# Kernel optimization log

Measured on AMD Instinct MI355X. Metric: run time of the kernel, lower is better.

Reference implementation:

```python
import jax, jax.numpy as jnp
import numpy as np

FRAME_LENGTH = 512
HOP_LENGTH = 256
ENERGY_THRESHOLD = 0.01
SAMPLE_RATE = 16000
SILENCE_FRAMES = int(0.3 * SAMPLE_RATE / HOP_LENGTH)      # 18
MIN_SPEECH_FRAMES = int(0.1 * SAMPLE_RATE / HOP_LENGTH)   # 6


def setup_inputs() -> dict:
    key = jax.random.key(0)
    waveform = jax.random.normal(key, (32, 960000), dtype=jnp.float32)
    return {"waveform": waveform}


def _compute_energy(waveform):
    # (B, S) -> (B, T): short-time mean-square energy, full frames only
    n = waveform.shape[-1]
    num_frames = max(1, (n - FRAME_LENGTH) // HOP_LENGTH + 1)
    idx = jnp.arange(num_frames)[:, None] * HOP_LENGTH + jnp.arange(FRAME_LENGTH)[None, :]
    frames = waveform[:, idx]                     # (B, T, F)
    return jnp.mean(frames * frames, axis=-1)


def _threshold(e):
    # torch.quantile(non_zero, 0.2) with linear interpolation; fallback to fixed threshold
    n = e.shape[0]
    s = jnp.sort(e)
    nzero = jnp.sum(s <= 0)          # number of entries excluded by (> 0)
    nz = n - nzero                   # count of positive entries
    pos = 0.2 * (nz - 1).astype(jnp.float32)
    lo = jnp.floor(pos).astype(jnp.int32)
    hi = jnp.ceil(pos).astype(jnp.int32)
    frac = pos - lo.astype(jnp.float32)
    ilo = jnp.clip(nzero + lo, 0, n - 1)
    ihi = jnp.clip(nzero + hi, 0, n - 1)
    q = s[ilo] * (1.0 - frac) + s[ihi] * frac
    return jnp.where(nz > 0, q, jnp.float32(ENERGY_THRESHOLD))


def _vad_one(e):
    # Faithful scan-based version of the per-frame hysteresis state machine.
    n = e.shape[0]
    m = e > _threshold(e)

    def step(state, xs):
        in_sp, start, sil = state
        t, mt = xs
        start2 = jnp.where(mt & ~in_sp, t, start)
        sil2 = jnp.where(mt, jnp.int32(0), jnp.where(in_sp, sil + 1, sil))
        closed = (~mt) & in_sp & (sil2 >= SILENCE_FRAMES)
        end = t - sil2  # matches original: end = t - silence_count (exclusive)
        in_sp2 = jnp.where(mt, True, jnp.where(closed, False, in_sp))
        return (in_sp2, start2, sil2), (closed, start2, end)

    init = (jnp.bool_(False), jnp.int32(0), jnp.int32(0))
    (in_sp_f, start_f, _), (closed, starts, ends) = jax.lax.scan(
        step, init, (jnp.arange(n, dtype=jnp.int32), m))

    # trailing open segment -> (start, n)
    starts = jnp.concatenate([starts, start_f[None]])
    ends = jnp.concatenate([ends, jnp.full((1,), n, dtype=jnp.int32)])
    valid = jnp.concatenate([closed, in_sp_f[None]])
    valid = valid & ((ends - starts) >= MIN_SPEECH_FRAMES)

    # mark mask[start:end] = True via +1/-1 diff then cumsum (RLE)
    sentinel = n + 1
    idx_s = jnp.where(valid, jnp.clip(starts, 0, n), sentinel)
    idx_e = jnp.where(valid, jnp.clip(ends, 0, n), sentinel)
    d = jnp.zeros(n + 2, dtype=jnp.int32)
    d = d.at[idx_s].add(1).at[idx_e].add(-1)
    return jnp.cumsum(d)[:n] > 0


def reference(waveform):
    energy = _compute_energy(waveform)     # (B, T)
    return jax.vmap(_vad_one)(energy)      # (B, T) bool VAD mask
```

## Files before the change

kernel.cpp:

```cpp
#include <hip/hip_runtime.h>

#define NFRAMES 3749
#define NBLOCKS 3750
#define NSAMP   960000
#define NBATCH  32
#define NWORDS  59
#define SILENCE_FRAMES 18
#define MIN_SPEECH_FRAMES 6
#define MAXSEG  256

__global__ __launch_bounds__(256) void vad_block_sums(const float* __restrict__ wav,
                                                      double* __restrict__ bs) {
    int tid = threadIdx.x;
    const float* p = wav + (size_t)blockIdx.x * 4096 + tid * 16;
    double acc = 0.0;
    #pragma unroll
    for (int i = 0; i < 4; ++i) {
        float4 v = *(const float4*)(p + i * 4);
        acc += (double)(v.x * v.x);
        acc += (double)(v.y * v.y);
        acc += (double)(v.z * v.z);
        acc += (double)(v.w * v.w);
    }
    #pragma unroll
    for (int m = 1; m < 16; m <<= 1)
        acc += __shfl_xor(acc, m, 64);
    if ((tid & 15) == 0)
        bs[(size_t)blockIdx.x * 16 + (tid >> 4)] = acc;
}

__global__ __launch_bounds__(256) void vad_finish(const double* __restrict__ bs,
                                                  int* __restrict__ out) {
    __shared__ float eng[NFRAMES];
    __shared__ int hist4[4][256];
    __shared__ unsigned long long mw[NWORDS];
    __shared__ unsigned long long sw[NWORDS];
    __shared__ unsigned long long lw[NWORDS];
    __shared__ unsigned long long Sw[NWORDS];
    __shared__ unsigned long long Ew[NWORDS];
    __shared__ int wbS[NWORDS], wbL[NWORDS];
    __shared__ int startpos[MAXSEG], lastpos[MAXSEG];
    __shared__ int nzero_sh, nseg_sh;
    __shared__ unsigned sel_prefix_sh;
    __shared__ int sel_k_sh;
    __shared__ int cLE_sh;
    __shared__ unsigned minGT_sh;
    __shared__ float thr_sh;

    int b = blockIdx.x;
    int tid = threadIdx.x;
    int lane = tid & 63, wv = tid >> 6;
    const double* row = bs + (size_t)b * NBLOCKS;

    if (tid == 0) nzero_sh = 0;
    __syncthreads();

    unsigned ub[15];
    int nel = 0, myzero = 0;
    #pragma unroll
    for (int i = 0; i < 15; ++i) {
        int t = tid + (i << 8);
        if (t < NFRAMES) {
            double s = row[t] + row[t + 1];
            float e = (float)(s * (1.0 / 512.0));
            eng[t] = e;
            ub[nel++] = __float_as_uint(e);
            if (e <= 0.0f) myzero++;
        }
    }
    if (myzero) atomicAdd(&nzero_sh, myzero);
    __syncthreads();

    int nzero = nzero_sh;
    int nz = NFRAMES - nzero;

    if (nz > 0) {
        float pos = 0.2f * (float)(nz - 1);
        int lo = (int)floorf(pos), hi = (int)ceilf(pos);
        int rank_lo = min(max(nzero + lo, 0), NFRAMES - 1);
        int rank_hi = min(max(nzero + hi, 0), NFRAMES - 1);

        for (int i = tid; i < 1024; i += 256) ((int*)hist4)[i] = 0;
        if (tid == 0) { sel_prefix_sh = 0u; sel_k_sh = rank_lo; }
        __syncthreads();

        for (int shift = 24; shift >= 0; shift -= 8) {
            unsigned pref = sel_prefix_sh;
            unsigned pmask = (shift == 24) ? 0u : (0xFFFFFFFFu << (shift + 8));
            for (int j = 0; j < nel; ++j) {
                unsigned u = ub[j];
                if ((u & pmask) == (pref & pmask))
                    atomicAdd(&hist4[wv][(u >> shift) & 255], 1);
            }
            __syncthreads();
            if (wv == 0) {
                int bin0 = lane << 2;
                int4 h0 = *(const int4*)&hist4[0][bin0];
                int4 h1 = *(const int4*)&hist4[1][bin0];
                int4 h2 = *(const int4*)&hist4[2][bin0];
                int4 h3 = *(const int4*)&hist4[3][bin0];
                int h[4];
                h[0] = h0.x + h1.x + h2.x + h3.x;
                h[1] = h0.y + h1.y + h2.y + h3.y;
                h[2] = h0.z + h1.z + h2.z + h3.z;
                h[3] = h0.w + h1.w + h2.w + h3.w;
                int tot = h[0] + h[1] + h[2] + h[3];
                int inc = tot;
                #pragma unroll
                for (int off = 1; off < 64; off <<= 1) {
                    int y = __shfl_up(inc, off, 64);
                    if (lane >= off) inc += y;
                }
                int run = inc - tot;
                int k = sel_k_sh;
                #pragma unroll
                for (int j = 0; j < 4; ++j) {
                    if (k >= run && k < run + h[j]) {
                        sel_prefix_sh = pref | ((unsigned)(bin0 + j) << shift);
                        sel_k_sh = k - run;
                    }
                    run += h[j];
                }
            }
            __syncthreads();
            if (shift > 0) {
                for (int i = tid; i < 1024; i += 256) ((int*)hist4)[i] = 0;
            }
            __syncthreads();
        }

        unsigned vb = sel_prefix_sh;

        if (rank_hi != rank_lo) {
            if (tid == 0) { cLE_sh = 0; minGT_sh = 0xFFFFFFFFu; }
            __syncthreads();
            int c = 0;
            unsigned mg = 0xFFFFFFFFu;
            for (int j = 0; j < nel; ++j) {
                unsigned u = ub[j];
                if (u <= vb) c++;
                else mg = min(mg, u);
            }
            #pragma unroll
            for (int off = 32; off > 0; off >>= 1) {
                c += __shfl_xor(c, off, 64);
                mg = min(mg, (unsigned)__shfl_xor((int)mg, off, 64));
            }
            if (lane == 0) {
                atomicAdd(&cLE_sh, c);
                atomicMin(&minGT_sh, mg);
            }
            __syncthreads();
        }

        if (tid == 0) {
            float vlo = __uint_as_float(vb);
            float vhi;
            if (rank_hi == rank_lo) vhi = vlo;
            else vhi = (cLE_sh >= rank_lo + 2) ? vlo : __uint_as_float(minGT_sh);
            float frac = pos - (float)lo;
            thr_sh = vlo * (1.0f - frac) + vhi * frac;
        }
    } else {
        if (tid == 0) thr_sh = 0.01f;
    }
    __syncthreads();
    float thr = thr_sh;

    for (int wi = wv; wi < NWORDS; wi += 4) {
        int t = (wi << 6) + lane;
        bool p = (t < NFRAMES) && (eng[t] > thr);
        unsigned long long bm = __ballot(p);
        if (lane == 0) mw[wi] = bm;
    }
    __syncthreads();

    for (int wi = wv; wi < NWORDS; wi += 4) {
        unsigned long long W  = mw[wi];
        unsigned long long Wm = (wi > 0) ? mw[wi - 1] : 0ull;
        unsigned long long Wp = (wi + 1 < NWORDS) ? mw[wi + 1] : 0ull;
        int l = lane;
        bool mt = (W >> l) & 1ull;
        bool prev_any, next_any;
        if (l >= 18) {
            prev_any = ((W >> (l - 18)) & 0x3FFFFull) != 0ull;
        } else {
            unsigned long long lowpart = W & ((1ull << l) - 1ull);
            unsigned long long hipart  = Wm >> (46 + l);
            prev_any = (lowpart | hipart) != 0ull;
        }
        if (l <= 45) {
            next_any = ((W >> (l + 1)) & 0x3FFFFull) != 0ull;
        } else {
            unsigned long long a  = (l < 63) ? (W >> (l + 1)) : 0ull;
            unsigned long long bb = Wp & ((1ull << (l - 45)) - 1ull);
            next_any = (a | bb) != 0ull;
        }
        unsigned long long bS = __ballot(mt && !prev_any);
        unsigned long long bL = __ballot(mt && !next_any);
        if (lane == 0) { sw[wi] = bS; lw[wi] = bL; }
    }
    __syncthreads();

    if (tid < NWORDS) {
        int cS = 0, cL = 0;
        for (int j = 0; j < tid; ++j) { cS += __popcll(sw[j]); cL += __popcll(lw[j]); }
        wbS[tid] = cS; wbL[tid] = cL;
        if (tid == NWORDS - 1) nseg_sh = cS + __popcll(sw[tid]);
    }
    __syncthreads();

    for (int wi = wv; wi < NWORDS; wi += 4) {
        unsigned long long wS = sw[wi], wL = lw[wi];
        int t = (wi << 6) + lane;
        unsigned long long lmask = (1ull << lane) - 1ull;
        if ((wS >> lane) & 1ull) startpos[wbS[wi] + __popcll(wS & lmask)] = t;
        if ((wL >> lane) & 1ull) lastpos[wbL[wi] + __popcll(wL & lmask)] = t;
    }
    for (int wi = tid; wi < NWORDS; wi += 256) { Sw[wi] = 0ull; Ew[wi] = 0ull; }
    __syncthreads();

    int nseg = nseg_sh;
    for (int k = tid; k < nseg; k += 256) {
        int s = startpos[k], L = lastpos[k];
        int e = (L >= NFRAMES - SILENCE_FRAMES) ? NFRAMES : L;
        if (e - s >= MIN_SPEECH_FRAMES) {
            atomicOr(&Sw[s >> 6], 1ull << (s & 63));
            atomicOr(&Ew[e >> 6], 1ull << (e & 63));
        }
    }
    __syncthreads();

    if (tid < NWORDS) {
        int cS = 0, cE = 0;
        for (int j = 0; j < tid; ++j) { cS += __popcll(Sw[j]); cE += __popcll(Ew[j]); }
        wbS[tid] = cS; wbL[tid] = cE;
    }
    __syncthreads();

    int* orow = out + (size_t)b * NFRAMES;
    for (int wi = wv; wi < NWORDS; wi += 4) {
        unsigned long long wS2 = Sw[wi], wE2 = Ew[wi];
        int t = (wi << 6) + lane;
        unsigned long long ile = (lane == 63) ? ~0ull : ((1ull << (lane + 1)) - 1ull);
        int cS = wbS[wi] + __popcll(wS2 & ile);
        int cE = wbL[wi] + __popcll(wE2 & ile);
        if (t < NFRAMES) orow[t] = (cS > cE) ? 1 : 0;
    }
}

extern "C" void kernel_launch(void* const* d_in, const int* in_sizes, int n_in,
                              void* d_out, int out_size, void* d_ws, size_t ws_size,
                              hipStream_t stream) {
    const float* wav = (const float*)d_in[0];
    int* out = (int*)d_out;
    double* bs = (double*)d_ws;

    vad_block_sums<<<(NBATCH * NSAMP) / 4096, 256, 0, stream>>>(wav, bs);
    vad_finish<<<NBATCH, 256, 0, stream>>>(bs, out);
}
```

Baseline: 197.5 us.

## Coalesce block-sum loads and widen finish kernel with per-pass histograms

The block-sum kernel now reads float4s in a fully coalesced stride across the block and reduces each 256-sample block with a full-wave shuffle. The finish kernel moves to 512 threads and keeps energies in registers instead of shared memory. It gives each radix-select pass its own per-wave histogram, so the zeroing barriers go away, and aggregates atomics when all lanes in a wave hit the same bin. Serial popcount prefix loops become wave-level scans. The intent is to cut latency in the single-block-per-batch finish stage and improve memory coalescing, at the cost of more shared memory and extra ballots per radix-select element.

```diff
diff --git a/kernel.cpp b/kernel.cpp
--- a/kernel.cpp
+++ b/kernel.cpp
@@ -12,27 +12,24 @@
 __global__ __launch_bounds__(256) void vad_block_sums(const float* __restrict__ wav,
                                                       double* __restrict__ bs) {
     int tid = threadIdx.x;
-    const float* p = wav + (size_t)blockIdx.x * 4096 + tid * 16;
-    double acc = 0.0;
+    int w = tid >> 6, lane = tid & 63;
+    const float4* q = (const float4*)(wav + (size_t)blockIdx.x * 4096);
     #pragma unroll
     for (int i = 0; i < 4; ++i) {
-        float4 v = *(const float4*)(p + i * 4);
-        acc += (double)(v.x * v.x);
-        acc += (double)(v.y * v.y);
-        acc += (double)(v.z * v.z);
-        acc += (double)(v.w * v.w);
-    }
-    #pragma unroll
-    for (int m = 1; m < 16; m <<= 1)
-        acc += __shfl_xor(acc, m, 64);
-    if ((tid & 15) == 0)
-        bs[(size_t)blockIdx.x * 16 + (tid >> 4)] = acc;
+        float4 v = q[(i << 8) + tid];
+        double a = (double)(v.x * v.x) + (double)(v.y * v.y)
+                 + (double)(v.z * v.z) + (double)(v.w * v.w);
+        #pragma unroll
+        for (int m = 1; m < 64; m <<= 1)
+            a += __shfl_xor(a, m, 64);
+        if (lane == 0)
+            bs[(size_t)blockIdx.x * 16 + (i << 2) + w] = a;
+    }
 }
 
-__global__ __launch_bounds__(256) void vad_finish(const double* __restrict__ bs,
+__global__ __launch_bounds__(512) void vad_finish(const double* __restrict__ bs,
                                                   int* __restrict__ out) {
-    __shared__ float eng[NFRAMES];
-    __shared__ int hist4[4][256];
+    __shared__ __attribute__((aligned(16))) int hist[4][8][256];
     __shared__ unsigned long long mw[NWORDS];
     __shared__ unsigned long long sw[NWORDS];
     __shared__ unsigned long long lw[NWORDS];
@@ -52,23 +49,29 @@
     int lane = tid & 63, wv = tid >> 6;
     const double* row = bs + (size_t)b * NBLOCKS;
 
-    if (tid == 0) nzero_sh = 0;
-    __syncthreads();
-
-    unsigned ub[15];
-    int nel = 0, myzero = 0;
-    #pragma unroll
-    for (int i = 0; i < 15; ++i) {
-        int t = tid + (i << 8);
+    if (tid == 0) { nzero_sh = 0; sel_prefix_sh = 0u; cLE_sh = 0; minGT_sh = 0xFFFFFFFFu; }
+    #pragma unroll
+    for (int i = 0; i < 4; ++i)
+        ((int4*)hist)[(i << 9) + tid] = make_int4(0, 0, 0, 0);
+
+    unsigned ub[8];
+    int myzero = 0;
+    #pragma unroll
+    for (int i = 0; i < 8; ++i) {
+        int t = tid + (i << 9);
+        unsigned u = 0xFFFFFFFFu;
         if (t < NFRAMES) {
             double s = row[t] + row[t + 1];
             float e = (float)(s * (1.0 / 512.0));
-            eng[t] = e;
-            ub[nel++] = __float_as_uint(e);
+            u = __float_as_uint(e);
             if (e <= 0.0f) myzero++;
         }
-    }
-    if (myzero) atomicAdd(&nzero_sh, myzero);
+        ub[i] = u;
+    }
+    #pragma unroll
+    for (int m = 1; m < 64; m <<= 1)
+        myzero += __shfl_xor(myzero, m, 64);
+    if (lane == 0 && myzero) atomicAdd(&nzero_sh, myzero);
     __syncthreads();
 
     int nzero = nzero_sh;
@@ -79,32 +82,40 @@
         int lo = (int)floorf(pos), hi = (int)ceilf(pos);
         int rank_lo = min(max(nzero + lo, 0), NFRAMES - 1);
         int rank_hi = min(max(nzero + hi, 0), NFRAMES - 1);
-
-        for (int i = tid; i < 1024; i += 256) ((int*)hist4)[i] = 0;
-        if (tid == 0) { sel_prefix_sh = 0u; sel_k_sh = rank_lo; }
-        __syncthreads();
-
-        for (int shift = 24; shift >= 0; shift -= 8) {
+        if (tid == 0) sel_k_sh = rank_lo;
+
+        int pno = 0;
+        for (int shift = 24; shift >= 0; shift -= 8, ++pno) {
             unsigned pref = sel_prefix_sh;
             unsigned pmask = (shift == 24) ? 0u : (0xFFFFFFFFu << (shift + 8));
-            for (int j = 0; j < nel; ++j) {
+            int* hw = hist[pno][wv];
+            #pragma unroll
+            for (int j = 0; j < 8; ++j) {
                 unsigned u = ub[j];
-                if ((u & pmask) == (pref & pmask))
-                    atomicAdd(&hist4[wv][(u >> shift) & 255], 1);
+                bool act = ((int)u >= 0) && ((u & pmask) == (pref & pmask));
+                unsigned long long ball = __ballot(act);
+                if (ball != 0ull) {
+                    unsigned bin = (u >> shift) & 255u;
+                    int leader = (int)__ffsll(ball) - 1;
+                    unsigned fbin = (unsigned)__shfl((int)bin, leader, 64);
+                    unsigned long long same = __ballot(act && (bin == fbin));
+                    if (same == ball) {
+                        if (lane == leader) atomicAdd(&hw[fbin], (int)__popcll(ball));
+                    } else if (act) {
+                        atomicAdd(&hw[bin], 1);
+                    }
+                }
             }
             __syncthreads();
             if (wv == 0) {
                 int bin0 = lane << 2;
-                int4 h0 = *(const int4*)&hist4[0][bin0];
-                int4 h1 = *(const int4*)&hist4[1][bin0];
-                int4 h2 = *(const int4*)&hist4[2][bin0];
-                int4 h3 = *(const int4*)&hist4[3][bin0];
-                int h[4];
-                h[0] = h0.x + h1.x + h2.x + h3.x;
-                h[1] = h0.y + h1.y + h2.y + h3.y;
-                h[2] = h0.z + h1.z + h2.z + h3.z;
-                h[3] = h0.w + h1.w + h2.w + h3.w;
-                int tot = h[0] + h[1] + h[2] + h[3];
+                int h0 = 0, h1 = 0, h2 = 0, h3 = 0;
+                #pragma unroll
+                for (int c = 0; c < 8; ++c) {
+                    int4 hc = *(const int4*)&hist[pno][c][bin0];
+                    h0 += hc.x; h1 += hc.y; h2 += hc.z; h3 += hc.w;
+                }
+                int tot = h0 + h1 + h2 + h3;
                 int inc = tot;
                 #pragma unroll
                 for (int off = 1; off < 64; off <<= 1) {
@@ -113,33 +124,31 @@
                 }
                 int run = inc - tot;
                 int k = sel_k_sh;
+                int hh[4] = {h0, h1, h2, h3};
                 #pragma unroll
-                for (int j = 0; j < 4; ++j) {
-                    if (k >= run && k < run + h[j]) {
-                        sel_prefix_sh = pref | ((unsigned)(bin0 + j) << shift);
+                for (int j2 = 0; j2 < 4; ++j2) {
+                    if (k >= run && k < run + hh[j2]) {
+                        sel_prefix_sh = pref | ((unsigned)(bin0 + j2) << shift);
                         sel_k_sh = k - run;
                     }
-                    run += h[j];
+                    run += hh[j2];
                 }
             }
             __syncthreads();
-            if (shift > 0) {
-                for (int i = tid; i < 1024; i += 256) ((int*)hist4)[i] = 0;
-            }
-            __syncthreads();
         }
 
         unsigned vb = sel_prefix_sh;
 
         if (rank_hi != rank_lo) {
-            if (tid == 0) { cLE_sh = 0; minGT_sh = 0xFFFFFFFFu; }
-            __syncthreads();
             int c = 0;
             unsigned mg = 0xFFFFFFFFu;
-            for (int j = 0; j < nel; ++j) {
+            #pragma unroll
+            for (int j = 0; j < 8; ++j) {
                 unsigned u = ub[j];
-                if (u <= vb) c++;
-                else mg = min(mg, u);
+                if ((int)u >= 0) {
+                    if (u <= vb) c++;
+                    else mg = min(mg, u);
+                }
             }
             #pragma unroll
             for (int off = 32; off > 0; off >>= 1) {
@@ -167,15 +176,17 @@
     __syncthreads();
     float thr = thr_sh;
 
-    for (int wi = wv; wi < NWORDS; wi += 4) {
-        int t = (wi << 6) + lane;
-        bool p = (t < NFRAMES) && (eng[t] > thr);
+    #pragma unroll
+    for (int i = 0; i < 8; ++i) {
+        unsigned u = ub[i];
+        bool p = ((int)u >= 0) && (__uint_as_float(u) > thr);
         unsigned long long bm = __ballot(p);
-        if (lane == 0) mw[wi] = bm;
-    }
-    __syncthreads();
-
-    for (int wi = wv; wi < NWORDS; wi += 4) {
+        int wi = wv + (i << 3);
+        if (lane == 0 && wi < NWORDS) mw[wi] = bm;
+    }
+    __syncthreads();
+
+    for (int wi = wv; wi < NWORDS; wi += 8) {
         unsigned long long W  = mw[wi];
         unsigned long long Wm = (wi > 0) ? mw[wi - 1] : 0ull;
         unsigned long long Wp = (wi + 1 < NWORDS) ? mw[wi + 1] : 0ull;
@@ -202,26 +213,34 @@
     }
     __syncthreads();
 
-    if (tid < NWORDS) {
-        int cS = 0, cL = 0;
-        for (int j = 0; j < tid; ++j) { cS += __popcll(sw[j]); cL += __popcll(lw[j]); }
-        wbS[tid] = cS; wbL[tid] = cL;
-        if (tid == NWORDS - 1) nseg_sh = cS + __popcll(sw[tid]);
-    }
-    __syncthreads();
-
-    for (int wi = wv; wi < NWORDS; wi += 4) {
+    if (wv < 2) {
+        const unsigned long long* src = (wv == 0) ? sw : lw;
+        unsigned long long w_ = (lane < NWORDS) ? src[lane] : 0ull;
+        int c = __popcll(w_);
+        int inc = c;
+        #pragma unroll
+        for (int off = 1; off < 64; off <<= 1) {
+            int y = __shfl_up(inc, off, 64);
+            if (lane >= off) inc += y;
+        }
+        int* dst = (wv == 0) ? wbS : wbL;
+        if (lane < NWORDS) dst[lane] = inc - c;
+        if (wv == 0 && lane == NWORDS - 1) nseg_sh = inc;
+    }
+    __syncthreads();
+
+    for (int wi = wv; wi < NWORDS; wi += 8) {
         unsigned long long wS = sw[wi], wL = lw[wi];
         int t = (wi << 6) + lane;
         unsigned long long lmask = (1ull << lane) - 1ull;
         if ((wS >> lane) & 1ull) startpos[wbS[wi] + __popcll(wS & lmask)] = t;
         if ((wL >> lane) & 1ull) lastpos[wbL[wi] + __popcll(wL & lmask)] = t;
     }
-    for (int wi = tid; wi < NWORDS; wi += 256) { Sw[wi] = 0ull; Ew[wi] = 0ull; }
+    for (int wi = tid; wi < NWORDS; wi += 512) { Sw[wi] = 0ull; Ew[wi] = 0ull; }
     __syncthreads();
 
     int nseg = nseg_sh;
-    for (int k = tid; k < nseg; k += 256) {
+    for (int k = tid; k < nseg; k += 512) {
         int s = startpos[k], L = lastpos[k];
         int e = (L >= NFRAMES - SILENCE_FRAMES) ? NFRAMES : L;
         if (e - s >= MIN_SPEECH_FRAMES) {
@@ -231,15 +250,23 @@
     }
     __syncthreads();
 
-    if (tid < NWORDS) {
-        int cS = 0, cE = 0;
-        for (int j = 0; j < tid; ++j) { cS += __popcll(Sw[j]); cE += __popcll(Ew[j]); }
-        wbS[tid] = cS; wbL[tid] = cE;
+    if (wv < 2) {
+        const unsigned long long* src = (wv == 0) ? Sw : Ew;
+        unsigned long long w_ = (lane < NWORDS) ? src[lane] : 0ull;
+        int c = __popcll(w_);
+        int inc = c;
+        #pragma unroll
+        for (int off = 1; off < 64; off <<= 1) {
+            int y = __shfl_up(inc, off, 64);
+            if (lane >= off) inc += y;
+        }
+        int* dst = (wv == 0) ? wbS : wbL;
+        if (lane < NWORDS) dst[lane] = inc - c;
     }
     __syncthreads();
 
     int* orow = out + (size_t)b * NFRAMES;
-    for (int wi = wv; wi < NWORDS; wi += 4) {
+    for (int wi = wv; wi < NWORDS; wi += 8) {
         unsigned long long wS2 = Sw[wi], wE2 = Ew[wi];
         int t = (wi << 6) + lane;
         unsigned long long ile = (lane == 63) ? ~0ull : ((1ull << (lane + 1)) - 1ull);
@@ -257,5 +284,5 @@
     double* bs = (double*)d_ws;
 
     vad_block_sums<<<(NBATCH * NSAMP) / 4096, 256, 0, stream>>>(wav, bs);
-    vad_finish<<<NBATCH, 256, 0, stream>>>(bs, out);
+    vad_finish<<<NBATCH, 512, 0, stream>>>(bs, out);
 }
```

New measurement: 185.2 us. 6.2% less time.
